# Kernel optimization log

Measured on AMD Instinct MI355X. Metric: run time of the kernel, lower is better.

Reference implementation:

```python
import jax, jax.numpy as jnp
import numpy as np

B, S, D, H = 4, 2048, 512, 8
HD = D // H  # 64


def setup_inputs() -> dict:
    key = jax.random.key(0)
    ks = jax.random.split(key, 7)
    scale = 1.0 / np.sqrt(D)
    return {
        "query": jax.random.normal(ks[0], (B, S, D), jnp.float32),
        "key": jax.random.normal(ks[1], (B, S, D), jnp.float32),
        "value": jax.random.normal(ks[2], (B, S, D), jnp.float32),
        # Only the `query` Linear and fc_out are actually used in the original forward
        "Wq": jax.random.uniform(ks[3], (D, D), jnp.float32, -scale, scale),
        "bq": jnp.zeros((D,), jnp.float32),
        "Wo": jax.random.uniform(ks[4], (D, D), jnp.float32, -scale, scale),
        "bo": jnp.zeros((D,), jnp.float32),
    }


def reference(query, key, value, Wq, bq, Wo, bo):
    # Faithful to source: Q, K, V all use the *query* projection (bug preserved)
    def proj(x):
        # [B,S,D] -> [B,H,S,HD]
        y = x @ Wq + bq
        return y.reshape(B, S, H, HD).transpose(0, 2, 1, 3)

    Q, K, V = proj(query), proj(key), proj(value)
    scores = jnp.einsum("bhqd,bhkd->bhqk", Q, K) / jnp.sqrt(jnp.float32(HD))
    attn = jax.nn.softmax(scores, axis=-1)
    x = jnp.einsum("bhqk,bhkd->bhqd", attn, V)
    x = x.transpose(0, 2, 1, 3).reshape(B, S, D)
    return x @ Wo + bo
```

## Files before the change

kernel.cpp:

```cpp
#include <hip/hip_runtime.h>
#include <math.h>

#define B_ 4
#define S_ 2048
#define D_ 512
#define H_ 8
#define HD_ 64
#define SZ_ (B_ * S_ * D_)
#define WSZ_ (D_ * D_)
#define BSH_ (B_ * S_ * H_)

#define QSCALE_ 0.18033688011112042f

typedef _Float16 v4h __attribute__((ext_vector_type(4)));
typedef _Float16 v8h __attribute__((ext_vector_type(8)));
typedef float    v4f __attribute__((ext_vector_type(4)));

__device__ __forceinline__ void gload16(const void* g, void* l) {
    __builtin_amdgcn_global_load_lds((__attribute__((address_space(1))) void*)g,
                                     (__attribute__((address_space(3))) void*)l,
                                     16, 0, 0);
}

__device__ __forceinline__ v8h pack8(v4f a, v4f b) {
    return __builtin_shufflevector(__builtin_convertvector(a, v4h),
                                   __builtin_convertvector(b, v4h),
                                   0, 1, 2, 3, 4, 5, 6, 7);
}

__global__ __launch_bounds__(256) void wtrans_kernel(const float* __restrict__ Wq,
                                                     const float* __restrict__ Wo,
                                                     _Float16* __restrict__ Wt) {
    __shared__ float Ts[64][132];
    const int kc = blockIdx.x, nt = blockIdx.y, mat = blockIdx.z;
    const float* W = mat ? Wo : Wq;
    const int k0 = kc * 64, n0 = nt * 128;
    const int t = threadIdx.x;
#pragma unroll
    for (int i = 0; i < 8; i++) {
        int s2 = t + i * 256;
        int kk = s2 >> 5, nc = (s2 & 31) * 4;
        *(float4*)&Ts[kk][nc] = *(const float4*)&W[(size_t)(k0 + kk) * 512 + n0 + nc];
    }
    __syncthreads();
    _Float16* blk = Wt + (((size_t)mat * 4 + nt) * 8 + kc) * 8192;
#pragma unroll
    for (int i = 0; i < 4; i++) {
        int s2 = t + i * 256;
        int r = s2 >> 3, s = s2 & 7;
        int kl = (s ^ (r & 7)) * 8;
        v8h p;
#pragma unroll
        for (int j = 0; j < 8; j++) p[j] = (_Float16)Ts[kl + j][r];
        *(v8h*)&blk[r * 64 + s * 8] = p;
    }
}

__global__ __launch_bounds__(256) void proj_mfma(const float* __restrict__ q,
                                                 const float* __restrict__ kin,
                                                 const float* __restrict__ v,
                                                 const _Float16* __restrict__ Wt,
                                                 const float* __restrict__ bq,
                                                 _Float16* __restrict__ Qh,
                                                 _Float16* __restrict__ Kh,
                                                 _Float16* __restrict__ VT) {
    __shared__ __align__(16) float    As[128 * 64];
    __shared__ __align__(16) _Float16 Bs[8192];
    const int blk = blockIdx.x;
    const int wl = (blk & 7) * 96 + (blk >> 3);
    const int z = wl >> 8;
    const int rem = wl & 255;
    const int mt = rem >> 2, nt = rem & 3;
    const int n0 = nt * 128, m0 = mt * 128;
    const float* X = (z == 0) ? q : ((z == 1) ? kin : v);
    const int t = threadIdx.x, lane = t & 63, w = t >> 6;
    const int wm = w >> 1, wn = w & 1;
    const int quad = lane >> 4, l16 = lane & 15;

    const _Float16* Bb = Wt + ((size_t)nt * 8) * 8192 + w * 512 + lane * 8;
    _Float16* Bd = Bs + w * 512;
    const float* Asrc[8];
#pragma unroll
    for (int i = 0; i < 8; i++) {
        int r = (w * 8 + i) * 4 + quad;
        int ch = l16 ^ (r & 7);
        Asrc[i] = X + (size_t)(m0 + r) * 512 + ch * 4;
    }
    float* Adst = As + w * 2048;

    v4f acc[4][4];
#pragma unroll
    for (int mi = 0; mi < 4; mi++)
#pragma unroll
        for (int ni = 0; ni < 4; ni++) acc[mi][ni] = (v4f)0.f;

    for (int kc = 0; kc < 8; ++kc) {
        __syncthreads();
#pragma unroll
        for (int i = 0; i < 8; i++)
            gload16(Asrc[i] + kc * 64, Adst + i * 256);
#pragma unroll
        for (int i = 0; i < 4; i++)
            gload16(Bb + kc * 8192 + i * 2048, Bd + i * 2048);
        __syncthreads();

#pragma unroll
        for (int ks = 0; ks < 2; ++ks) {
            const int sxx = (ks * 32 + quad * 8) ^ ((l16 & 7) * 8);
            const int c0 = ks * 8 + quad * 2;
            v8h af[4], bf[4];
#pragma unroll
            for (int mi = 0; mi < 4; mi++) {
                const int R = wm * 64 + mi * 16 + l16;
                v4f lo = *(const v4f*)&As[R * 64 + ((c0 ^ (R & 7)) * 4)];
                v4f hi = *(const v4f*)&As[R * 64 + (((c0 + 1) ^ (R & 7)) * 4)];
                af[mi] = pack8(lo, hi);
            }
#pragma unroll
            for (int ni = 0; ni < 4; ni++)
                bf[ni] = *(const v8h*)&Bs[(wn * 64 + ni * 16 + l16) * 64 + sxx];
#pragma unroll
            for (int mi = 0; mi < 4; mi++)
#pragma unroll
                for (int ni = 0; ni < 4; ni++)
                    acc[mi][ni] = __builtin_amdgcn_mfma_f32_16x16x32_f16(af[mi], bf[ni], acc[mi][ni], 0, 0, 0);
        }
    }

    if (z < 2) {
        _Float16* Y = z ? Kh : Qh;
        const float sc = z ? 1.f : QSCALE_;
#pragma unroll
        for (int mi = 0; mi < 4; mi++) {
            int mb = m0 + wm * 64 + mi * 16 + quad * 4;
#pragma unroll
            for (int ni = 0; ni < 4; ni++) {
                int n = n0 + wn * 64 + ni * 16 + l16;
                float bj = bq[n];
#pragma unroll
                for (int r = 0; r < 4; r++)
                    Y[(size_t)(mb + r) * 512 + n] = (_Float16)((acc[mi][ni][r] + bj) * sc);
            }
        }
    } else {
#pragma unroll
        for (int mi = 0; mi < 4; mi++) {
            int tile0 = (m0 & 2047) + wm * 64;
            int pos = tile0 + (mi >> 1) * 32 + quad * 8 + (mi & 1) * 4;
            int b = m0 >> 11;
#pragma unroll
            for (int ni = 0; ni < 4; ni++) {
                int n = n0 + wn * 64 + ni * 16 + l16;
                int h = n >> 6, dd = n & 63;
                float bj = bq[n];
                v4h pk;
#pragma unroll
                for (int r = 0; r < 4; r++) pk[r] = (_Float16)(acc[mi][ni][r] + bj);
                *(v4h*)&VT[(((size_t)b * H_ + h) * HD_ + dd) * S_ + pos] = pk;
            }
        }
    }
}

__global__ __launch_bounds__(256) void outproj_mfma(const _Float16* __restrict__ Ah,
                                                    const _Float16* __restrict__ Wt,
                                                    const float* __restrict__ bo,
                                                    float* __restrict__ out) {
    __shared__ __align__(16) _Float16 As[8192];
    __shared__ __align__(16) _Float16 Bs[8192];
    const int blk = blockIdx.x;
    const int wl = (blk & 7) * 32 + (blk >> 3);
    const int mt = wl >> 2, nt = wl & 3;
    const int n0 = nt * 128, m0 = mt * 128;
    const int t = threadIdx.x, lane = t & 63, w = t >> 6;
    const int wm = w >> 1, wn = w & 1;
    const int quad = lane >> 4, l16 = lane & 15;

    const _Float16* Ab = Ah + ((size_t)mt * 8) * 8192 + w * 512 + lane * 8;
    const _Float16* Bb = Wt + (size_t)(4 + nt) * 8 * 8192 + w * 512 + lane * 8;
    _Float16* Ad = As + w * 512;
    _Float16* Bd = Bs + w * 512;

    v4f acc[4][4];
#pragma unroll
    for (int mi = 0; mi < 4; mi++)
#pragma unroll
        for (int ni = 0; ni < 4; ni++) acc[mi][ni] = (v4f)0.f;

    for (int kc = 0; kc < 8; ++kc) {
        __syncthreads();
#pragma unroll
        for (int i = 0; i < 4; i++) {
            gload16(Ab + kc * 8192 + i * 2048, Ad + i * 2048);
            gload16(Bb + kc * 8192 + i * 2048, Bd + i * 2048);
        }
        __syncthreads();

#pragma unroll
        for (int ks = 0; ks < 2; ++ks) {
            const int sxx = (ks * 32 + quad * 8) ^ ((l16 & 7) * 8);
            v8h af[4], bf[4];
#pragma unroll
            for (int mi = 0; mi < 4; mi++)
                af[mi] = *(const v8h*)&As[(wm * 64 + mi * 16 + l16) * 64 + sxx];
#pragma unroll
            for (int ni = 0; ni < 4; ni++)
                bf[ni] = *(const v8h*)&Bs[(wn * 64 + ni * 16 + l16) * 64 + sxx];
#pragma unroll
            for (int mi = 0; mi < 4; mi++)
#pragma unroll
                for (int ni = 0; ni < 4; ni++)
                    acc[mi][ni] = __builtin_amdgcn_mfma_f32_16x16x32_f16(af[mi], bf[ni], acc[mi][ni], 0, 0, 0);
        }
    }

#pragma unroll
    for (int mi = 0; mi < 4; mi++) {
        int mb = m0 + wm * 64 + mi * 16 + quad * 4;
#pragma unroll
        for (int ni = 0; ni < 4; ni++) {
            int n = n0 + wn * 64 + ni * 16 + l16;
            float bj = bo[n];
#pragma unroll
            for (int r = 0; r < 4; r++)
                out[(size_t)(mb + r) * 512 + n] = acc[mi][ni][r] + bj;
        }
    }
}

__global__ __launch_bounds__(256) void flash_attn_f16(const _Float16* __restrict__ Qh,
                                                      const _Float16* __restrict__ Kh,
                                                      const _Float16* __restrict__ VT,
                                                      _Float16* __restrict__ Ah) {
    __shared__ _Float16 Ks[128 * 72];
    __shared__ _Float16 Vs[64 * 136];

    const int t     = threadIdx.x;
    const int lane  = t & 63;
    const int w     = t >> 6;
    const int quad  = lane >> 4;
    const int l16   = lane & 15;
    const int blk = blockIdx.x;
    const int xcd = blk & 7, idx = blk >> 3;
    const int pid = xcd * 4 + (idx >> 4);
    const int qb  = idx & 15;
    const int b   = pid >> 3, h = pid & 7;
    const int q0  = qb * 128;

    const size_t base  = (size_t)b * S_ * D_ + (size_t)h * HD_;
    const size_t vbase = ((size_t)b * H_ + h) * HD_ * (size_t)S_;

    v8h qf[2][2];
#pragma unroll
    for (int nb = 0; nb < 2; nb++) {
        const _Float16* qrow = Qh + base + (size_t)(q0 + w * 32 + nb * 16 + l16) * D_;
        qf[nb][0] = *(const v8h*)(qrow + quad * 8);
        qf[nb][1] = *(const v8h*)(qrow + 32 + quad * 8);
    }

    v4f o[2][4];
#pragma unroll
    for (int nb = 0; nb < 2; nb++)
#pragma unroll
        for (int i = 0; i < 4; i++) o[nb][i] = (v4f)0.f;
    float l_lane[2] = {0.f, 0.f};

    v8h kv[4], vv[4];
#define LOADKV(kk)                                                             \
    do {                                                                       \
        _Pragma("unroll") for (int i = 0; i < 4; i++) {                        \
            int c = t + i * 256;                                               \
            kv[i] = *(const v8h*)(Kh + base + (size_t)((kk) + (c >> 3)) * D_ + (c & 7) * 8); \
            vv[i] = *(const v8h*)(VT + vbase + (size_t)(c >> 4) * S_ + (kk) + (c & 15) * 8); \
        }                                                                      \
    } while (0)

    LOADKV(0);

    for (int kk0 = 0; kk0 < S_; kk0 += 128) {
        __syncthreads();
#pragma unroll
        for (int i = 0; i < 4; i++) {
            int c = t + i * 256;
            *(v8h*)&Ks[(c >> 3) * 72 + (c & 7) * 8] = kv[i];
            *(v8h*)&Vs[(c >> 4) * 136 + (c & 15) * 8] = vv[i];
        }
        __syncthreads();

        if (kk0 + 128 < S_) LOADKV(kk0 + 128);

#pragma unroll
        for (int hh = 0; hh < 2; hh++) {
            v4f sc[4][2];
#pragma unroll
            for (int mb = 0; mb < 4; mb++)
#pragma unroll
                for (int nb = 0; nb < 2; nb++) sc[mb][nb] = (v4f)0.f;
#pragma unroll
            for (int ks = 0; ks < 2; ks++) {
#pragma unroll
                for (int mb = 0; mb < 4; mb++) {
                    v8h ak = *(const v8h*)&Ks[(hh * 64 + mb * 16 + l16) * 72 + ks * 32 + quad * 8];
#pragma unroll
                    for (int nb = 0; nb < 2; nb++)
                        sc[mb][nb] = __builtin_amdgcn_mfma_f32_16x16x32_f16(ak, qf[nb][ks], sc[mb][nb], 0, 0, 0);
                }
            }

            v4h pf[4][2];
#pragma unroll
            for (int nb = 0; nb < 2; nb++) {
#pragma unroll
                for (int mb = 0; mb < 4; mb++) {
                    v4f pv;
#pragma unroll
                    for (int r = 0; r < 4; r++) pv[r] = __builtin_amdgcn_exp2f(sc[mb][nb][r]);
                    pf[mb][nb] = __builtin_convertvector(pv, v4h);
                    l_lane[nb] += (pv[0] + pv[1]) + (pv[2] + pv[3]);
                }
            }

#pragma unroll
            for (int p = 0; p < 2; p++) {
#pragma unroll
                for (int dblk = 0; dblk < 4; dblk++) {
                    v8h vf2 = *(const v8h*)&Vs[(dblk * 16 + l16) * 136 + hh * 64 + p * 32 + quad * 8];
                    v4h vlo = __builtin_shufflevector(vf2, vf2, 0, 1, 2, 3);
                    v4h vhi = __builtin_shufflevector(vf2, vf2, 4, 5, 6, 7);
#pragma unroll
                    for (int nb = 0; nb < 2; nb++) {
                        o[nb][dblk] = __builtin_amdgcn_mfma_f32_16x16x16f16(vlo, pf[2 * p][nb], o[nb][dblk], 0, 0, 0);
                        o[nb][dblk] = __builtin_amdgcn_mfma_f32_16x16x16f16(vhi, pf[2 * p + 1][nb], o[nb][dblk], 0, 0, 0);
                    }
                }
            }
        }
    }
#undef LOADKV

#pragma unroll
    for (int nb = 0; nb < 2; nb++) {
        float rs = l_lane[nb];
        rs += __shfl_xor(rs, 16);
        rs += __shfl_xor(rs, 32);
        float linv = __builtin_amdgcn_rcpf(rs);
        int r = w * 32 + nb * 16 + l16;
        _Float16* blkp = Ah + (((size_t)(b * 16 + qb)) * 8 + h) * 8192 + r * 64;
#pragma unroll
        for (int dblk = 0; dblk < 4; dblk++) {
            int s = dblk * 2 + (quad >> 1);
            v4h pk;
#pragma unroll
            for (int rr = 0; rr < 4; rr++) pk[rr] = (_Float16)(o[nb][dblk][rr] * linv);
            *(v4h*)&blkp[((s ^ (r & 7)) * 8) + (quad & 1) * 4] = pk;
        }
    }
}

extern "C" void kernel_launch(void* const* d_in, const int* in_sizes, int n_in,
                              void* d_out, int out_size, void* d_ws, size_t ws_size,
                              hipStream_t stream) {
    const float* query = (const float*)d_in[0];
    const float* key   = (const float*)d_in[1];
    const float* value = (const float*)d_in[2];
    const float* Wq    = (const float*)d_in[3];
    const float* bq    = (const float*)d_in[4];
    const float* Wo    = (const float*)d_in[5];
    const float* bo    = (const float*)d_in[6];
    float* out = (float*)d_out;

    _Float16* ws = (_Float16*)d_ws;
    _Float16* Qh = ws;
    _Float16* Kh = ws + (size_t)SZ_;
    _Float16* VT = ws + 2 * (size_t)SZ_;
    _Float16* Wt = ws + 3 * (size_t)SZ_;
    _Float16* Ah = ws + 3 * (size_t)SZ_ + 2 * (size_t)WSZ_;

    wtrans_kernel<<<dim3(8, 4, 2), 256, 0, stream>>>(Wq, Wo, Wt);
    proj_mfma<<<dim3(768), 256, 0, stream>>>(query, key, value, Wt, bq, Qh, Kh, VT);
    flash_attn_f16<<<dim3(512), 256, 0, stream>>>(Qh, Kh, VT, Ah);
    outproj_mfma<<<dim3(256), 256, 0, stream>>>(Ah, Wt, bo, out);
}
```

Baseline: 190.9 us.

## Double-buffer LDS tiles in projection GEMMs and convert activations to fp16 on staging

Both projection GEMM kernels now use two LDS buffers per operand, so loads for the next K chunk are issued before computing on the current one, with one barrier per iteration instead of two. The input projection also stops staging fp32 activations via direct-to-LDS loads. It register-prefetches them two chunks ahead, packs them to fp16 and stores a swizzled fp16 tile, so the inner loop reads fp16 fragments directly. This trades more LDS per block and more registers for latency hiding and smaller LDS traffic.

```diff
diff --git a/kernel.cpp b/kernel.cpp
--- a/kernel.cpp
+++ b/kernel.cpp
@@ -64,8 +64,8 @@
                                                  _Float16* __restrict__ Qh,
                                                  _Float16* __restrict__ Kh,
                                                  _Float16* __restrict__ VT) {
-    __shared__ __align__(16) float    As[128 * 64];
-    __shared__ __align__(16) _Float16 Bs[8192];
+    __shared__ __align__(16) _Float16 As[2][8192];
+    __shared__ __align__(16) _Float16 Bs[2][8192];
     const int blk = blockIdx.x;
     const int wl = (blk & 7) * 96 + (blk >> 3);
     const int z = wl >> 8;
@@ -77,16 +77,16 @@
     const int wm = w >> 1, wn = w & 1;
     const int quad = lane >> 4, l16 = lane & 15;
 
+    const float* Ap[4];
+    int wofs[4];
+#pragma unroll
+    for (int i = 0; i < 4; i++) {
+        int s2 = t + i * 256;
+        int r = s2 >> 3, c = s2 & 7;
+        Ap[i] = X + (size_t)(m0 + r) * 512 + c * 8;
+        wofs[i] = r * 64 + ((c ^ (r & 7)) * 8);
+    }
     const _Float16* Bb = Wt + ((size_t)nt * 8) * 8192 + w * 512 + lane * 8;
-    _Float16* Bd = Bs + w * 512;
-    const float* Asrc[8];
-#pragma unroll
-    for (int i = 0; i < 8; i++) {
-        int r = (w * 8 + i) * 4 + quad;
-        int ch = l16 ^ (r & 7);
-        Asrc[i] = X + (size_t)(m0 + r) * 512 + ch * 4;
-    }
-    float* Adst = As + w * 2048;
 
     v4f acc[4][4];
 #pragma unroll
@@ -94,37 +94,60 @@
 #pragma unroll
         for (int ni = 0; ni < 4; ni++) acc[mi][ni] = (v4f)0.f;
 
+    v4f a0[4], a1[4];
+#pragma unroll
+    for (int i = 0; i < 4; i++) {
+        a0[i] = *(const v4f*)(Ap[i]);
+        a1[i] = *(const v4f*)(Ap[i] + 4);
+    }
+#pragma unroll
+    for (int i = 0; i < 4; i++) *(v8h*)&As[0][wofs[i]] = pack8(a0[i], a1[i]);
+#pragma unroll
+    for (int i = 0; i < 4; i++)
+        gload16(Bb + i * 2048, &Bs[0][w * 512 + i * 2048]);
+#pragma unroll
+    for (int i = 0; i < 4; i++) {
+        a0[i] = *(const v4f*)(Ap[i] + 64);
+        a1[i] = *(const v4f*)(Ap[i] + 68);
+    }
+    __syncthreads();
+
+    int cur = 0;
     for (int kc = 0; kc < 8; ++kc) {
-        __syncthreads();
-#pragma unroll
-        for (int i = 0; i < 8; i++)
-            gload16(Asrc[i] + kc * 64, Adst + i * 256);
-#pragma unroll
-        for (int i = 0; i < 4; i++)
-            gload16(Bb + kc * 8192 + i * 2048, Bd + i * 2048);
-        __syncthreads();
+        const int nxt = cur ^ 1;
+        if (kc + 1 < 8) {
+#pragma unroll
+            for (int i = 0; i < 4; i++) *(v8h*)&As[nxt][wofs[i]] = pack8(a0[i], a1[i]);
+#pragma unroll
+            for (int i = 0; i < 4; i++)
+                gload16(Bb + (kc + 1) * 8192 + i * 2048, &Bs[nxt][w * 512 + i * 2048]);
+        }
+        if (kc + 2 < 8) {
+#pragma unroll
+            for (int i = 0; i < 4; i++) {
+                a0[i] = *(const v4f*)(Ap[i] + (kc + 2) * 64);
+                a1[i] = *(const v4f*)(Ap[i] + (kc + 2) * 64 + 4);
+            }
+        }
 
 #pragma unroll
         for (int ks = 0; ks < 2; ++ks) {
             const int sxx = (ks * 32 + quad * 8) ^ ((l16 & 7) * 8);
-            const int c0 = ks * 8 + quad * 2;
             v8h af[4], bf[4];
 #pragma unroll
-            for (int mi = 0; mi < 4; mi++) {
-                const int R = wm * 64 + mi * 16 + l16;
-                v4f lo = *(const v4f*)&As[R * 64 + ((c0 ^ (R & 7)) * 4)];
-                v4f hi = *(const v4f*)&As[R * 64 + (((c0 + 1) ^ (R & 7)) * 4)];
-                af[mi] = pack8(lo, hi);
-            }
+            for (int mi = 0; mi < 4; mi++)
+                af[mi] = *(const v8h*)&As[cur][(wm * 64 + mi * 16 + l16) * 64 + sxx];
 #pragma unroll
             for (int ni = 0; ni < 4; ni++)
-                bf[ni] = *(const v8h*)&Bs[(wn * 64 + ni * 16 + l16) * 64 + sxx];
+                bf[ni] = *(const v8h*)&Bs[cur][(wn * 64 + ni * 16 + l16) * 64 + sxx];
 #pragma unroll
             for (int mi = 0; mi < 4; mi++)
 #pragma unroll
                 for (int ni = 0; ni < 4; ni++)
                     acc[mi][ni] = __builtin_amdgcn_mfma_f32_16x16x32_f16(af[mi], bf[ni], acc[mi][ni], 0, 0, 0);
         }
+        __syncthreads();
+        cur = nxt;
     }
 
     if (z < 2) {
@@ -166,8 +189,8 @@
                                                     const _Float16* __restrict__ Wt,
                                                     const float* __restrict__ bo,
                                                     float* __restrict__ out) {
-    __shared__ __align__(16) _Float16 As[8192];
-    __shared__ __align__(16) _Float16 Bs[8192];
+    __shared__ __align__(16) _Float16 As[2][8192];
+    __shared__ __align__(16) _Float16 Bs[2][8192];
     const int blk = blockIdx.x;
     const int wl = (blk & 7) * 32 + (blk >> 3);
     const int mt = wl >> 2, nt = wl & 3;
@@ -178,8 +201,6 @@
 
     const _Float16* Ab = Ah + ((size_t)mt * 8) * 8192 + w * 512 + lane * 8;
     const _Float16* Bb = Wt + (size_t)(4 + nt) * 8 * 8192 + w * 512 + lane * 8;
-    _Float16* Ad = As + w * 512;
-    _Float16* Bd = Bs + w * 512;
 
     v4f acc[4][4];
 #pragma unroll
@@ -187,14 +208,23 @@
 #pragma unroll
         for (int ni = 0; ni < 4; ni++) acc[mi][ni] = (v4f)0.f;
 
+#pragma unroll
+    for (int i = 0; i < 4; i++) {
+        gload16(Ab + i * 2048, &As[0][w * 512 + i * 2048]);
+        gload16(Bb + i * 2048, &Bs[0][w * 512 + i * 2048]);
+    }
+    __syncthreads();
+
+    int cur = 0;
     for (int kc = 0; kc < 8; ++kc) {
-        __syncthreads();
-#pragma unroll
-        for (int i = 0; i < 4; i++) {
-            gload16(Ab + kc * 8192 + i * 2048, Ad + i * 2048);
-            gload16(Bb + kc * 8192 + i * 2048, Bd + i * 2048);
-        }
-        __syncthreads();
+        const int nxt = cur ^ 1;
+        if (kc + 1 < 8) {
+#pragma unroll
+            for (int i = 0; i < 4; i++) {
+                gload16(Ab + (kc + 1) * 8192 + i * 2048, &As[nxt][w * 512 + i * 2048]);
+                gload16(Bb + (kc + 1) * 8192 + i * 2048, &Bs[nxt][w * 512 + i * 2048]);
+            }
+        }
 
 #pragma unroll
         for (int ks = 0; ks < 2; ++ks) {
@@ -202,16 +232,18 @@
             v8h af[4], bf[4];
 #pragma unroll
             for (int mi = 0; mi < 4; mi++)
-                af[mi] = *(const v8h*)&As[(wm * 64 + mi * 16 + l16) * 64 + sxx];
+                af[mi] = *(const v8h*)&As[cur][(wm * 64 + mi * 16 + l16) * 64 + sxx];
 #pragma unroll
             for (int ni = 0; ni < 4; ni++)
-                bf[ni] = *(const v8h*)&Bs[(wn * 64 + ni * 16 + l16) * 64 + sxx];
+                bf[ni] = *(const v8h*)&Bs[cur][(wn * 64 + ni * 16 + l16) * 64 + sxx];
 #pragma unroll
             for (int mi = 0; mi < 4; mi++)
 #pragma unroll
                 for (int ni = 0; ni < 4; ni++)
                     acc[mi][ni] = __builtin_amdgcn_mfma_f32_16x16x32_f16(af[mi], bf[ni], acc[mi][ni], 0, 0, 0);
         }
+        __syncthreads();
+        cur = nxt;
     }
 
 #pragma unroll
```

Measured after the change: 186.5 us. 2.3% less time.
